# Performance work log

Hardware: AMD Instinct MI355X
Metric: run time of the kernel (lower is better)

The kernel has to match this reference:

```python
import jax, jax.numpy as jnp
import numpy as np

B, S, E, F = 64, 8192, 8, 32  # batch, seq, embed_dim(=n_qubits), ffn_dim


def setup_inputs() -> dict:
    key = jax.random.key(0)
    k_x, k_t, k_w1, k_b1, k_w2, k_b2 = jax.random.split(key, 6)
    x = jax.random.normal(k_x, (B, S, E), dtype=jnp.float32)
    theta = jax.random.normal(k_t, (E,), dtype=jnp.float32)  # trainable RX angles
    lim1 = 1.0 / np.sqrt(E)
    lim2 = 1.0 / np.sqrt(F)
    w1 = jax.random.uniform(k_w1, (E, F), jnp.float32, -lim1, lim1)
    b1 = jax.random.uniform(k_b1, (F,), jnp.float32, -lim1, lim1)
    w2 = jax.random.uniform(k_w2, (F, E), jnp.float32, -lim2, lim2)
    b2 = jax.random.uniform(k_b2, (E,), jnp.float32, -lim2, lim2)
    return {"x": x, "theta": theta, "w1": w1, "b1": b1, "w2": w2, "b2": b2}


def reference(x, theta, w1, b1, w2, b2):
    # Quantum circuit: per wire i, RX(x_i) then RX(theta_i) on |0>, measure PauliZ.
    # Single-qubit RX gates compose: <Z> after RX(phi)|0> = cos(phi). Wires are
    # independent (no entangling gates), so MeasureAll(PauliZ) = cos(x + theta).
    q_out = jnp.cos(x + theta)                      # [B, S, E]
    h = jax.nn.relu(q_out @ w1 + b1)                # [B, S, F]
    return h @ w2 + b2                              # [B, S, E]
```

## Files before the change

### kernel.cpp

```cpp
#include <hip/hip_runtime.h>


#define TPB 256
#define TOKT 4

__global__ __launch_bounds__(TPB) void ffq_kernel(
    const float4* __restrict__ xv,
    const float*  __restrict__ theta,
    const float*  __restrict__ w1,
    const float*  __restrict__ b1,
    const float*  __restrict__ w2,
    const float*  __restrict__ b2,
    float4*       __restrict__ outv,
    int ntok)
{
    __shared__ float wc[32 * 16];
    __shared__ float sb1[32];
    __shared__ float sth[8];
    __shared__ float sb2[8];

    const int tid = threadIdx.x;
    {
        int e = tid >> 5, f = tid & 31;
        wc[f * 16 + e] = w1[tid];
        int f2 = tid >> 3, e2 = tid & 7;
        wc[f2 * 16 + 8 + e2] = w2[tid];
    }
    if (tid < 32) sb1[tid] = b1[tid];
    if (tid < 8)  { sth[tid] = theta[tid]; sb2[tid] = b2[tid]; }
    __syncthreads();

    float th[8], bb2[8];
#pragma unroll
    for (int e = 0; e < 8; ++e) { th[e] = sth[e]; bb2[e] = sb2[e]; }

    const long base   = (long)blockIdx.x * TPB + tid;
    const long stride = (long)gridDim.x * TPB;

    float q[TOKT][8];
    float o[TOKT][8];

#pragma unroll
    for (int t = 0; t < TOKT; ++t) {
        long g = base + (long)t * stride;
        if (g < ntok) {
            float4 a = xv[2 * g];
            float4 c = xv[2 * g + 1];
            q[t][0] = __cosf(a.x + th[0]);
            q[t][1] = __cosf(a.y + th[1]);
            q[t][2] = __cosf(a.z + th[2]);
            q[t][3] = __cosf(a.w + th[3]);
            q[t][4] = __cosf(c.x + th[4]);
            q[t][5] = __cosf(c.y + th[5]);
            q[t][6] = __cosf(c.z + th[6]);
            q[t][7] = __cosf(c.w + th[7]);
        } else {
#pragma unroll
            for (int e = 0; e < 8; ++e) q[t][e] = 0.0f;
        }
#pragma unroll
        for (int e = 0; e < 8; ++e) o[t][e] = bb2[e];
    }

#pragma unroll 4
    for (int f = 0; f < 32; ++f) {
        const float4* wr = (const float4*)(&wc[f * 16]);
        const float4 wa  = wr[0];
        const float4 wb  = wr[1];
        const float4 va  = wr[2];
        const float4 vb  = wr[3];
        const float  bb  = sb1[f];
#pragma unroll
        for (int t = 0; t < TOKT; ++t) {
            float h = bb;
            h = fmaf(q[t][0], wa.x, h);
            h = fmaf(q[t][1], wa.y, h);
            h = fmaf(q[t][2], wa.z, h);
            h = fmaf(q[t][3], wa.w, h);
            h = fmaf(q[t][4], wb.x, h);
            h = fmaf(q[t][5], wb.y, h);
            h = fmaf(q[t][6], wb.z, h);
            h = fmaf(q[t][7], wb.w, h);
            h = fmaxf(h, 0.0f);
            o[t][0] = fmaf(h, va.x, o[t][0]);
            o[t][1] = fmaf(h, va.y, o[t][1]);
            o[t][2] = fmaf(h, va.z, o[t][2]);
            o[t][3] = fmaf(h, va.w, o[t][3]);
            o[t][4] = fmaf(h, vb.x, o[t][4]);
            o[t][5] = fmaf(h, vb.y, o[t][5]);
            o[t][6] = fmaf(h, vb.z, o[t][6]);
            o[t][7] = fmaf(h, vb.w, o[t][7]);
        }
    }

#pragma unroll
    for (int t = 0; t < TOKT; ++t) {
        long g = base + (long)t * stride;
        if (g < ntok) {
            outv[2 * g]     = make_float4(o[t][0], o[t][1], o[t][2], o[t][3]);
            outv[2 * g + 1] = make_float4(o[t][4], o[t][5], o[t][6], o[t][7]);
        }
    }
}

extern "C" void kernel_launch(void* const* d_in, const int* in_sizes, int n_in,
                              void* d_out, int out_size, void* d_ws, size_t ws_size,
                              hipStream_t stream) {
    const float* x     = (const float*)d_in[0];
    const float* theta = (const float*)d_in[1];
    const float* w1    = (const float*)d_in[2];
    const float* b1    = (const float*)d_in[3];
    const float* w2    = (const float*)d_in[4];
    const float* b2    = (const float*)d_in[5];
    float* out = (float*)d_out;

    const int ntok = in_sizes[0] / 8;
    const int total_threads = (ntok + TOKT - 1) / TOKT;
    const int grid = (total_threads + TPB - 1) / TPB;

    ffq_kernel<<<grid, TPB, 0, stream>>>(
        (const float4*)x, theta, w1, b1, w2, b2, (float4*)out, ntok);
}
```

Before: 84.10 us.

## Drop shared-memory weight staging and read uniform weights directly from global

Removes the LDS staging of weights, biases and theta and the block barrier, and instead reads the uniform weight arrays straight from global memory inside a fully unrolled hidden loop, where the compiler can turn them into scalar loads. Tokens per thread drop from 4 to 2, launch bounds request higher occupancy, indices switch to 32-bit, and all x loads are issued before the cosines. The goal is to cut LDS traffic and the barrier and to hide memory latency through more resident waves. In exchange it relies on scalar-cache hits for the weights and does less arithmetic reuse per thread.

```diff
diff --git a/kernel.cpp b/kernel.cpp
--- a/kernel.cpp
+++ b/kernel.cpp
@@ -2,9 +2,9 @@
 
 
 #define TPB 256
-#define TOKT 4
+#define TOKT 2
 
-__global__ __launch_bounds__(TPB) void ffq_kernel(
+__global__ __launch_bounds__(TPB, 4) void ffq_kernel(
     const float4* __restrict__ xv,
     const float*  __restrict__ theta,
     const float*  __restrict__ w1,
@@ -14,88 +14,61 @@
     float4*       __restrict__ outv,
     int ntok)
 {
-    __shared__ float wc[32 * 16];
-    __shared__ float sb1[32];
-    __shared__ float sth[8];
-    __shared__ float sb2[8];
-
-    const int tid = threadIdx.x;
-    {
-        int e = tid >> 5, f = tid & 31;
-        wc[f * 16 + e] = w1[tid];
-        int f2 = tid >> 3, e2 = tid & 7;
-        wc[f2 * 16 + 8 + e2] = w2[tid];
-    }
-    if (tid < 32) sb1[tid] = b1[tid];
-    if (tid < 8)  { sth[tid] = theta[tid]; sb2[tid] = b2[tid]; }
-    __syncthreads();
-
-    float th[8], bb2[8];
-#pragma unroll
-    for (int e = 0; e < 8; ++e) { th[e] = sth[e]; bb2[e] = sb2[e]; }
-
-    const long base   = (long)blockIdx.x * TPB + tid;
-    const long stride = (long)gridDim.x * TPB;
+    const int base   = blockIdx.x * TPB + threadIdx.x;
+    const int stride = gridDim.x * TPB;
 
     float q[TOKT][8];
     float o[TOKT][8];
 
+    float4 a[TOKT], c[TOKT];
 #pragma unroll
     for (int t = 0; t < TOKT; ++t) {
-        long g = base + (long)t * stride;
+        int g = base + t * stride;
         if (g < ntok) {
-            float4 a = xv[2 * g];
-            float4 c = xv[2 * g + 1];
-            q[t][0] = __cosf(a.x + th[0]);
-            q[t][1] = __cosf(a.y + th[1]);
-            q[t][2] = __cosf(a.z + th[2]);
-            q[t][3] = __cosf(a.w + th[3]);
-            q[t][4] = __cosf(c.x + th[4]);
-            q[t][5] = __cosf(c.y + th[5]);
-            q[t][6] = __cosf(c.z + th[6]);
-            q[t][7] = __cosf(c.w + th[7]);
+            a[t] = xv[2 * g];
+            c[t] = xv[2 * g + 1];
         } else {
-#pragma unroll
-            for (int e = 0; e < 8; ++e) q[t][e] = 0.0f;
-        }
-#pragma unroll
-        for (int e = 0; e < 8; ++e) o[t][e] = bb2[e];
-    }
-
-#pragma unroll 4
-    for (int f = 0; f < 32; ++f) {
-        const float4* wr = (const float4*)(&wc[f * 16]);
-        const float4 wa  = wr[0];
-        const float4 wb  = wr[1];
-        const float4 va  = wr[2];
-        const float4 vb  = wr[3];
-        const float  bb  = sb1[f];
-#pragma unroll
-        for (int t = 0; t < TOKT; ++t) {
-            float h = bb;
-            h = fmaf(q[t][0], wa.x, h);
-            h = fmaf(q[t][1], wa.y, h);
-            h = fmaf(q[t][2], wa.z, h);
-            h = fmaf(q[t][3], wa.w, h);
-            h = fmaf(q[t][4], wb.x, h);
-            h = fmaf(q[t][5], wb.y, h);
-            h = fmaf(q[t][6], wb.z, h);
-            h = fmaf(q[t][7], wb.w, h);
-            h = fmaxf(h, 0.0f);
-            o[t][0] = fmaf(h, va.x, o[t][0]);
-            o[t][1] = fmaf(h, va.y, o[t][1]);
-            o[t][2] = fmaf(h, va.z, o[t][2]);
-            o[t][3] = fmaf(h, va.w, o[t][3]);
-            o[t][4] = fmaf(h, vb.x, o[t][4]);
-            o[t][5] = fmaf(h, vb.y, o[t][5]);
-            o[t][6] = fmaf(h, vb.z, o[t][6]);
-            o[t][7] = fmaf(h, vb.w, o[t][7]);
+            a[t] = make_float4(0.f, 0.f, 0.f, 0.f);
+            c[t] = make_float4(0.f, 0.f, 0.f, 0.f);
         }
     }
 
 #pragma unroll
     for (int t = 0; t < TOKT; ++t) {
-        long g = base + (long)t * stride;
+        q[t][0] = __cosf(a[t].x + theta[0]);
+        q[t][1] = __cosf(a[t].y + theta[1]);
+        q[t][2] = __cosf(a[t].z + theta[2]);
+        q[t][3] = __cosf(a[t].w + theta[3]);
+        q[t][4] = __cosf(c[t].x + theta[4]);
+        q[t][5] = __cosf(c[t].y + theta[5]);
+        q[t][6] = __cosf(c[t].z + theta[6]);
+        q[t][7] = __cosf(c[t].w + theta[7]);
+#pragma unroll
+        for (int e = 0; e < 8; ++e) o[t][e] = b2[e];
+    }
+
+#pragma unroll
+    for (int f = 0; f < 32; ++f) {
+        const float bb = b1[f];
+        float wa[8], wb[8];
+#pragma unroll
+        for (int e = 0; e < 8; ++e) wa[e] = w1[e * 32 + f];
+#pragma unroll
+        for (int e = 0; e < 8; ++e) wb[e] = w2[f * 8 + e];
+#pragma unroll
+        for (int t = 0; t < TOKT; ++t) {
+            float h = bb;
+#pragma unroll
+            for (int e = 0; e < 8; ++e) h = fmaf(q[t][e], wa[e], h);
+            h = fmaxf(h, 0.0f);
+#pragma unroll
+            for (int e = 0; e < 8; ++e) o[t][e] = fmaf(h, wb[e], o[t][e]);
+        }
+    }
+
+#pragma unroll
+    for (int t = 0; t < TOKT; ++t) {
+        int g = base + t * stride;
         if (g < ntok) {
             outv[2 * g]     = make_float4(o[t][0], o[t][1], o[t][2], o[t][3]);
             outv[2 * g + 1] = make_float4(o[t][4], o[t][5], o[t][6], o[t][7]);
```

New measurement: 123.1 us. 46.4% more time.

## Double tokens per thread, prefetch inputs before barrier, software-pipeline weight loads

Applied to the files above, without the earlier changes.

Raises tokens per thread from 4 to 8 and issues all global loads of x before the shared-memory barrier, so the weight staging overlaps with input fetch. Theta and b2 are now read directly from global memory instead of shared memory, and index arithmetic moves from 64-bit to 32-bit. The FFN loop is fully unrolled and prefetches the next row of weights from LDS while the current row is used. These changes add register pressure (64 q/o values plus 16 float4 inputs per thread), which may lower occupancy, and the grid shrinks by half.

```diff
diff --git a/kernel.cpp b/kernel.cpp
--- a/kernel.cpp
+++ b/kernel.cpp
@@ -2,7 +2,7 @@
 
 
 #define TPB 256
-#define TOKT 4
+#define TOKT 8
 
 __global__ __launch_bounds__(TPB) void ffq_kernel(
     const float4* __restrict__ xv,
@@ -16,8 +16,6 @@
 {
     __shared__ float wc[32 * 16];
     __shared__ float sb1[32];
-    __shared__ float sth[8];
-    __shared__ float sb2[8];
 
     const int tid = threadIdx.x;
     {
@@ -27,49 +25,60 @@
         wc[f2 * 16 + 8 + e2] = w2[tid];
     }
     if (tid < 32) sb1[tid] = b1[tid];
-    if (tid < 8)  { sth[tid] = theta[tid]; sb2[tid] = b2[tid]; }
-    __syncthreads();
 
     float th[8], bb2[8];
 #pragma unroll
-    for (int e = 0; e < 8; ++e) { th[e] = sth[e]; bb2[e] = sb2[e]; }
+    for (int e = 0; e < 8; ++e) { th[e] = theta[e]; bb2[e] = b2[e]; }
 
-    const long base   = (long)blockIdx.x * TPB + tid;
-    const long stride = (long)gridDim.x * TPB;
+    const int base   = blockIdx.x * TPB + tid;
+    const int stride = gridDim.x * TPB;
+
+    float4 a[TOKT], c[TOKT];
+#pragma unroll
+    for (int t = 0; t < TOKT; ++t) {
+        int g = base + t * stride;
+        if (g < ntok) {
+            a[t] = xv[2 * g];
+            c[t] = xv[2 * g + 1];
+        } else {
+            a[t] = make_float4(0.f, 0.f, 0.f, 0.f);
+            c[t] = make_float4(0.f, 0.f, 0.f, 0.f);
+        }
+    }
+
+    __syncthreads();
 
     float q[TOKT][8];
     float o[TOKT][8];
-
 #pragma unroll
     for (int t = 0; t < TOKT; ++t) {
-        long g = base + (long)t * stride;
-        if (g < ntok) {
-            float4 a = xv[2 * g];
-            float4 c = xv[2 * g + 1];
-            q[t][0] = __cosf(a.x + th[0]);
-            q[t][1] = __cosf(a.y + th[1]);
-            q[t][2] = __cosf(a.z + th[2]);
-            q[t][3] = __cosf(a.w + th[3]);
-            q[t][4] = __cosf(c.x + th[4]);
-            q[t][5] = __cosf(c.y + th[5]);
-            q[t][6] = __cosf(c.z + th[6]);
-            q[t][7] = __cosf(c.w + th[7]);
-        } else {
-#pragma unroll
-            for (int e = 0; e < 8; ++e) q[t][e] = 0.0f;
-        }
+        q[t][0] = __cosf(a[t].x + th[0]);
+        q[t][1] = __cosf(a[t].y + th[1]);
+        q[t][2] = __cosf(a[t].z + th[2]);
+        q[t][3] = __cosf(a[t].w + th[3]);
+        q[t][4] = __cosf(c[t].x + th[4]);
+        q[t][5] = __cosf(c[t].y + th[5]);
+        q[t][6] = __cosf(c[t].z + th[6]);
+        q[t][7] = __cosf(c[t].w + th[7]);
 #pragma unroll
         for (int e = 0; e < 8; ++e) o[t][e] = bb2[e];
     }
 
-#pragma unroll 4
+    const float4* wcv = (const float4*)wc;
+    float4 wa = wcv[0], wb = wcv[1], va = wcv[2], vb = wcv[3];
+    float  bb = sb1[0];
+
+#pragma unroll
     for (int f = 0; f < 32; ++f) {
-        const float4* wr = (const float4*)(&wc[f * 16]);
-        const float4 wa  = wr[0];
-        const float4 wb  = wr[1];
-        const float4 va  = wr[2];
-        const float4 vb  = wr[3];
-        const float  bb  = sb1[f];
+        float4 nwa, nwb, nva, nvb;
+        float  nbb;
+        if (f < 31) {
+            nwa = wcv[4 * f + 4];
+            nwb = wcv[4 * f + 5];
+            nva = wcv[4 * f + 6];
+            nvb = wcv[4 * f + 7];
+            nbb = sb1[f + 1];
+        }
 #pragma unroll
         for (int t = 0; t < TOKT; ++t) {
             float h = bb;
@@ -91,11 +100,12 @@
             o[t][6] = fmaf(h, vb.z, o[t][6]);
             o[t][7] = fmaf(h, vb.w, o[t][7]);
         }
+        wa = nwa; wb = nwb; va = nva; vb = nvb; bb = nbb;
     }
 
 #pragma unroll
     for (int t = 0; t < TOKT; ++t) {
-        long g = base + (long)t * stride;
+        int g = base + t * stride;
         if (g < ntok) {
             outv[2 * g]     = make_float4(o[t][0], o[t][1], o[t][2], o[t][3]);
             outv[2 * g + 1] = make_float4(o[t][4], o[t][5], o[t][6], o[t][7]);
```

Result: slower. 185.7 us (+120.7%).
